# Performance work log

Measured on AMD Instinct MI355X. Metric: run time of the kernel, lower is better.

Reference implementation:

```python
import jax, jax.numpy as jnp
import numpy as np

TABLE_NUM = 16
TABLE_SIZE_LOG2 = 12
T = 1 << TABLE_SIZE_LOG2          # 4096 entries per table
FEAT = 2                          # features per entry (mini_linear in = table_num*2)
Z_DIM = 512
RES_MIN = 16
RES_MAX = 256
IMG = 256
MLP_HIDDEN = 64
OUT_DIM = 3
BATCH = 8
PRIME_Y = np.uint32(2654435761)   # instant-NGP spatial hash prime


def setup_inputs() -> dict:
    key = jax.random.key(0)
    ks = jax.random.split(key, 9)
    d_tab = TABLE_NUM * T * FEAT
    return {
        "z": jax.random.normal(ks[0], (BATCH, Z_DIM), jnp.float32),
        "w_table": jax.random.normal(ks[1], (Z_DIM, d_tab), jnp.float32) * 1e-2,
        "b_table": jnp.zeros((d_tab,), jnp.float32),
        "w1": jax.random.normal(ks[2], (TABLE_NUM * FEAT, MLP_HIDDEN), jnp.float32) * (1.0 / np.sqrt(TABLE_NUM * FEAT)),
        "b1": jnp.zeros((MLP_HIDDEN,), jnp.float32),
        "w2": jax.random.normal(ks[3], (MLP_HIDDEN, MLP_HIDDEN), jnp.float32) * (1.0 / np.sqrt(MLP_HIDDEN)),
        "b2": jnp.zeros((MLP_HIDDEN,), jnp.float32),
        "w3": jax.random.normal(ks[4], (MLP_HIDDEN, OUT_DIM), jnp.float32) * (1.0 / np.sqrt(MLP_HIDDEN)),
        "b3": jnp.zeros((OUT_DIM,), jnp.float32),
    }


def _sample_coords(b):
    c = (jnp.arange(IMG, dtype=jnp.float32) + 0.5) / IMG
    xx, yy = jnp.meshgrid(c, c, indexing="ij")  # torch.meshgrid default
    coords = jnp.stack([xx, yy], axis=-1).reshape(1, -1, 2)
    return jnp.broadcast_to(coords, (b, IMG * IMG, 2))


def _hash_retrieve(tables, coords):
    """tables: B x L x T x F; coords: B x N x 2 in [0,1). Returns B x N x (L*F)."""
    B, L, _, _ = tables.shape
    growth = np.exp((np.log(RES_MAX) - np.log(RES_MIN)) / (L - 1))
    offs = jnp.array([[0, 0], [1, 0], [0, 1], [1, 1]], dtype=jnp.uint32)  # 4 corners
    bidx = jnp.arange(B)[:, None, None]
    feats = []
    for l in range(L):
        res = jnp.float32(RES_MIN * (growth ** l))
        pos = coords * res                      # B,N,2
        pos0 = jnp.floor(pos)
        frac = pos - pos0                       # B,N,2
        corner = pos0.astype(jnp.uint32)[:, :, None, :] + offs[None, None]  # B,N,4,2
        idx = (corner[..., 0] ^ (corner[..., 1] * PRIME_Y)) & jnp.uint32(T - 1)
        f = tables[:, l][bidx, idx.astype(jnp.int32)]        # B,N,4,F gather
        fx, fy = frac[..., 0], frac[..., 1]
        w = jnp.stack([(1 - fx) * (1 - fy), fx * (1 - fy),
                       (1 - fx) * fy,       fx * fy], axis=-1)  # B,N,4
        feats.append(jnp.einsum("bncf,bnc->bnf", f, w))
    return jnp.concatenate(feats, axis=-1)


def reference(z, w_table, b_table, w1, b1, w2, b2, w3, b3):
    B = z.shape[0]
    tables = (z @ w_table + b_table).reshape(B, TABLE_NUM, T, FEAT)
    coords = _sample_coords(B).astype(tables.dtype)
    feat = _hash_retrieve(tables, coords)                    # B,N,L*F
    h = jax.nn.relu(feat @ w1 + b1)
    h = jax.nn.relu(h @ w2 + b2)
    o = jnp.tanh(h @ w3 + b3)                                # B,N,3
    return o.reshape(B, IMG, IMG, OUT_DIM).transpose(0, 3, 1, 2)
```

## Files before the change

kernel.cpp:

```cpp
#include <hip/hip_runtime.h>
#include <cmath>

#define TABLE_NUM 16
#define T_SIZE    4096
#define Z_DIM     512
#define IMG       256
#define D_TAB     (TABLE_NUM * T_SIZE * 2)
#define BATCH     8
#define HID       64
#define N_PIX     (IMG * IMG)
#define PRIME_Y   2654435761u
#define KCHUNK    4
#define KLEN      (Z_DIM / KCHUNK)
#define NG4       (D_TAB / 4)

typedef _Float16 v8h  __attribute__((ext_vector_type(8)));
typedef _Float16 v2h  __attribute__((ext_vector_type(2)));
typedef float    v4f  __attribute__((ext_vector_type(4)));

struct ResArr { float r[TABLE_NUM]; };

__device__ constexpr int WCAP[16]  = {3,4,4,4,5,5,5,6,7,8,9,10,11,13,15,18};
__device__ constexpr int CBASE[16] = {0,9,25,41,57,82,107,132,168,217,281,362,462,583,752,977};
#define CTOT 1301

__global__ void prep_weights(const float* __restrict__ w1, const float* __restrict__ w2,
                             const float* __restrict__ w3, const float* __restrict__ z,
                             _Float16* __restrict__ w1T, _Float16* __restrict__ w2T,
                             _Float16* __restrict__ w3T, float* __restrict__ zT)
{
    const int t = threadIdx.x;
    for (int i = t; i < HID * 32; i += 256) {
        int n = i >> 5, k = i & 31;
        w1T[i] = (_Float16)w1[k * HID + n];
    }
    for (int i = t; i < HID * HID; i += 256) {
        int n = i >> 6, k = i & 63;
        w2T[i] = (_Float16)w2[k * HID + n];
    }
    for (int i = t; i < 16 * HID; i += 256) {
        int n = i >> 6, k = i & 63;
        w3T[i] = (_Float16)(n < 3 ? w3[k * 3 + n] : 0.f);
    }
    for (int i = t; i < Z_DIM * BATCH; i += 256) {
        int k = i >> 3, b = i & 7;
        zT[i] = z[b * Z_DIM + k];
    }
}

__global__ __launch_bounds__(256) void gen_partial(
    const float* __restrict__ zT, const float* __restrict__ w,
    float* __restrict__ part)
{
    const int c  = blockIdx.x >> 7;
    const int g  = (blockIdx.x & 127) * 256 + threadIdx.x;
    const int k0 = c * KLEN;
    const float4* wp = reinterpret_cast<const float4*>(w) + g;

    float4 acc[BATCH];
#pragma unroll
    for (int b = 0; b < BATCH; ++b) acc[b] = make_float4(0.f, 0.f, 0.f, 0.f);

#pragma unroll 8
    for (int kk = 0; kk < KLEN; ++kk) {
        const int k = k0 + kk;
        float4 wv = wp[(size_t)k * NG4];
        const float* zr = zT + k * BATCH;
#pragma unroll
        for (int b = 0; b < BATCH; ++b) {
            float zv = zr[b];
            acc[b].x = fmaf(zv, wv.x, acc[b].x);
            acc[b].y = fmaf(zv, wv.y, acc[b].y);
            acc[b].z = fmaf(zv, wv.z, acc[b].z);
            acc[b].w = fmaf(zv, wv.w, acc[b].w);
        }
    }

    float4* pp = reinterpret_cast<float4*>(part);
#pragma unroll
    for (int b = 0; b < BATCH; ++b)
        pp[((size_t)(c * BATCH + b) << 15) + g] = acc[b];
}

__global__ __launch_bounds__(256) void gen_reduce(
    const float* __restrict__ part, const float* __restrict__ bt,
    float* __restrict__ tabs)
{
    const int i = blockIdx.x * 256 + threadIdx.x;
    const int b = i >> 15, g = i & (NG4 - 1);
    const float4* pp = reinterpret_cast<const float4*>(part);

    float4 s = pp[((size_t)b << 15) + g];
#pragma unroll
    for (int c = 1; c < KCHUNK; ++c) {
        float4 p = pp[((size_t)(c * BATCH + b) << 15) + g];
        s.x += p.x; s.y += p.y; s.z += p.z; s.w += p.w;
    }
    float4 bv = reinterpret_cast<const float4*>(bt)[g];
    s.x += bv.x; s.y += bv.y; s.z += bv.z; s.w += bv.w;
    reinterpret_cast<float4*>(tabs)[((size_t)b << 15) + g] = s;
}

__global__ __launch_bounds__(256) void hash_mlp(
    const float* __restrict__ tabs,
    const _Float16* __restrict__ w1T, const _Float16* __restrict__ w2T,
    const _Float16* __restrict__ w3T,
    const float* __restrict__ b1, const float* __restrict__ b2,
    const float* __restrict__ b3,
    float* __restrict__ out, ResArr res)
{
    __shared__ _Float16 mbuf[4][64][72];
    __shared__ float2   cstage[CTOT];

    const int tid  = threadIdx.x;
    const int wid  = tid >> 6;
    const int lane = tid & 63;
    const int b    = blockIdx.x & 7;
    const int tile = blockIdx.x >> 3;
    const int i0b  = (tile >> 4) * 16;
    const int j0b  = (tile & 15) * 16;
    const int i0   = i0b + wid * 4;

    const int di = lane >> 4, dj = lane & 15;
    const float cxp = ((float)(i0 + di) + 0.5f) * (1.0f / IMG);
    const float cyp = ((float)(j0b + dj) + 0.5f) * (1.0f / IMG);
    const float2* tb2 = reinterpret_cast<const float2*>(tabs + (size_t)b * D_TAB);

    const float cx_lo = ((float)i0b + 0.5f) * (1.0f / IMG);
    const float cy_lo = ((float)j0b + 0.5f) * (1.0f / IMG);

#pragma unroll
    for (int l = 0; l < TABLE_NUM; ++l) {
        const float r  = res.r[l];
        const int   xs = (int)floorf(cx_lo * r);
        const int   ys = (int)floorf(cy_lo * r);
        const float2* tl = tb2 + l * T_SIZE;
        const int W = WCAP[l], CNT = WCAP[l] * WCAP[l];
        for (int e = tid; e < CNT; e += 256) {
            int yy = e / W, xx = e - yy * W;
            unsigned idx = ((unsigned)(xs + xx) ^
                            ((unsigned)(ys + yy) * PRIME_Y)) & (T_SIZE - 1);
            cstage[CBASE[l] + e] = tl[idx];
        }
    }
    __syncthreads();

#pragma unroll
    for (int l = 0; l < TABLE_NUM; ++l) {
        const float r   = res.r[l];
        const float xsf = floorf(cx_lo * r);
        const float ysf = floorf(cy_lo * r);
        float px = cxp * r, py = cyp * r;
        float fx0 = floorf(px), fy0 = floorf(py);
        float fx = px - fx0, fy = py - fy0;
        int xi = (int)(fx0 - xsf), yi = (int)(fy0 - ysf);
        const float2* cb = cstage + CBASE[l];
        const int W = WCAP[l];
        float2 f00 = cb[yi * W + xi];
        float2 f10 = cb[yi * W + xi + 1];
        float2 f01 = cb[(yi + 1) * W + xi];
        float2 f11 = cb[(yi + 1) * W + xi + 1];
        float w00 = (1.f - fx) * (1.f - fy);
        float w10 = fx * (1.f - fy);
        float w01 = (1.f - fx) * fy;
        float w11 = fx * fy;
        float e0 = f00.x * w00 + f10.x * w10 + f01.x * w01 + f11.x * w11;
        float e1 = f00.y * w00 + f10.y * w10 + f01.y * w01 + f11.y * w11;
        v2h p; p.x = (_Float16)e0; p.y = (_Float16)e1;
        *reinterpret_cast<v2h*>(&mbuf[wid][lane][2 * l]) = p;
    }

    const int arow = lane & 15;
    const int kgrp = lane >> 4;

    float bias1v[4], bias2v[4];
#pragma unroll
    for (int nt = 0; nt < 4; ++nt) {
        bias1v[nt] = b1[nt * 16 + arow];
        bias2v[nt] = b2[nt * 16 + arow];
    }
    const float bias3 = (arow < 3) ? b3[arow] : 0.f;

    v8h bf1[4], bf2a[4], bf2b[4];
#pragma unroll
    for (int nt = 0; nt < 4; ++nt) {
        bf1[nt]  = *reinterpret_cast<const v8h*>(&w1T[(nt * 16 + arow) * 32 + kgrp * 8]);
        bf2a[nt] = *reinterpret_cast<const v8h*>(&w2T[(nt * 16 + arow) * 64 + kgrp * 8]);
        bf2b[nt] = *reinterpret_cast<const v8h*>(&w2T[(nt * 16 + arow) * 64 + 32 + kgrp * 8]);
    }
    v8h bf3a = *reinterpret_cast<const v8h*>(&w3T[arow * 64 + kgrp * 8]);
    v8h bf3b = *reinterpret_cast<const v8h*>(&w3T[arow * 64 + 32 + kgrp * 8]);

    v8h a1[4];
#pragma unroll
    for (int mt = 0; mt < 4; ++mt)
        a1[mt] = *reinterpret_cast<const v8h*>(&mbuf[wid][mt * 16 + arow][kgrp * 8]);

    v4f c1[4][4];
#pragma unroll
    for (int nt = 0; nt < 4; ++nt)
#pragma unroll
        for (int mt = 0; mt < 4; ++mt) {
            v4f c = {0.f, 0.f, 0.f, 0.f};
            c = __builtin_amdgcn_mfma_f32_16x16x32_f16(a1[mt], bf1[nt], c, 0, 0, 0);
#pragma unroll
            for (int e = 0; e < 4; ++e)
                c1[mt][nt][e] = fmaxf(c[e] + bias1v[nt], 0.f);
        }

#pragma unroll
    for (int mt = 0; mt < 4; ++mt)
#pragma unroll
        for (int nt = 0; nt < 4; ++nt)
#pragma unroll
            for (int e = 0; e < 4; ++e)
                mbuf[wid][mt * 16 + kgrp * 4 + e][nt * 16 + arow] = (_Float16)c1[mt][nt][e];

    v8h a2[4][2];
#pragma unroll
    for (int mt = 0; mt < 4; ++mt) {
        a2[mt][0] = *reinterpret_cast<const v8h*>(&mbuf[wid][mt * 16 + arow][kgrp * 8]);
        a2[mt][1] = *reinterpret_cast<const v8h*>(&mbuf[wid][mt * 16 + arow][32 + kgrp * 8]);
    }
    v4f c2[4][4];
#pragma unroll
    for (int nt = 0; nt < 4; ++nt)
#pragma unroll
        for (int mt = 0; mt < 4; ++mt) {
            v4f c = {0.f, 0.f, 0.f, 0.f};
            c = __builtin_amdgcn_mfma_f32_16x16x32_f16(a2[mt][0], bf2a[nt], c, 0, 0, 0);
            c = __builtin_amdgcn_mfma_f32_16x16x32_f16(a2[mt][1], bf2b[nt], c, 0, 0, 0);
#pragma unroll
            for (int e = 0; e < 4; ++e)
                c2[mt][nt][e] = fmaxf(c[e] + bias2v[nt], 0.f);
        }

#pragma unroll
    for (int mt = 0; mt < 4; ++mt)
#pragma unroll
        for (int nt = 0; nt < 4; ++nt)
#pragma unroll
            for (int e = 0; e < 4; ++e)
                mbuf[wid][mt * 16 + kgrp * 4 + e][nt * 16 + arow] = (_Float16)c2[mt][nt][e];

#pragma unroll
    for (int mt = 0; mt < 4; ++mt) {
        v8h a0  = *reinterpret_cast<const v8h*>(&mbuf[wid][mt * 16 + arow][kgrp * 8]);
        v8h a1v = *reinterpret_cast<const v8h*>(&mbuf[wid][mt * 16 + arow][32 + kgrp * 8]);
        v4f c = {0.f, 0.f, 0.f, 0.f};
        c = __builtin_amdgcn_mfma_f32_16x16x32_f16(a0,  bf3a, c, 0, 0, 0);
        c = __builtin_amdgcn_mfma_f32_16x16x32_f16(a1v, bf3b, c, 0, 0, 0);
        if (arow < 3) {
            float4 st;
            st.x = tanhf(c[0] + bias3);
            st.y = tanhf(c[1] + bias3);
            st.z = tanhf(c[2] + bias3);
            st.w = tanhf(c[3] + bias3);
            size_t idx = ((size_t)b * 3 + arow) * N_PIX
                       + (size_t)(i0 + mt) * IMG + j0b + kgrp * 4;
            *reinterpret_cast<float4*>(&out[idx]) = st;
        }
    }
}

extern "C" void kernel_launch(void* const* d_in, const int* in_sizes, int n_in,
                              void* d_out, int out_size, void* d_ws, size_t ws_size,
                              hipStream_t stream)
{
    const float* z  = (const float*)d_in[0];
    const float* wt = (const float*)d_in[1];
    const float* bt = (const float*)d_in[2];
    const float* w1 = (const float*)d_in[3];
    const float* b1 = (const float*)d_in[4];
    const float* w2 = (const float*)d_in[5];
    const float* b2 = (const float*)d_in[6];
    const float* w3 = (const float*)d_in[7];
    const float* b3 = (const float*)d_in[8];
    float* out  = (float*)d_out;

    char* ws = (char*)d_ws;
    float*     tabs = (float*)ws;
    float*     part = (float*)(ws + (4 << 20));
    _Float16*  w1T  = (_Float16*)(ws + (20 << 20));
    _Float16*  w2T  = (_Float16*)(ws + (20 << 20) + 4096);
    _Float16*  w3T  = (_Float16*)(ws + (20 << 20) + 12288);
    float*     zT   = (float*)(ws + (20 << 20) + 16384);

    ResArr ra;
    const double growth = std::exp((std::log(256.0) - std::log(16.0)) / 15.0);
    for (int l = 0; l < TABLE_NUM; ++l)
        ra.r[l] = (float)(16.0 * std::pow(growth, (double)l));

    prep_weights<<<1, 256, 0, stream>>>(w1, w2, w3, z, w1T, w2T, w3T, zT);
    gen_partial<<<KCHUNK * (NG4 / 256), 256, 0, stream>>>(zT, wt, part);
    gen_reduce<<<BATCH * NG4 / 256, 256, 0, stream>>>(part, bt, tabs);
    hash_mlp<<<BATCH * (N_PIX / 256), 256, 0, stream>>>(
        tabs, w1T, w2T, w3T, b1, b2, b3, out, ra);
}
```

Baseline: 99.41 us.

## Shrink hash_mlp tiles and swap MFMA operand roles with register shuffles

Each block now covers a 4x16 pixel tile, and each wave handles one 16-pixel row, so the grid is four times larger. The staged corner region is sized per level with separate x and y widths, which shrinks shared memory to a small cstage buffer. The MLP is rewritten to use weights as the A operand and per-pixel features as B. Intermediate activations move between layers through ds_bpermute in registers rather than an LDS mbuf round-trip. This removes the large shared buffer and its traffic, which should raise occupancy. The cost is more redundant table gathers across the smaller tiles, repeated weight loads per wave, and narrower scalar output stores.

After: 129.8 us. +30.6%, slower.

```diff
diff --git a/kernel.cpp b/kernel.cpp
--- a/kernel.cpp
+++ b/kernel.cpp
@@ -20,9 +20,15 @@
 
 struct ResArr { float r[TABLE_NUM]; };
 
-__device__ constexpr int WCAP[16]  = {3,4,4,4,5,5,5,6,7,8,9,10,11,13,15,18};
-__device__ constexpr int CBASE[16] = {0,9,25,41,57,82,107,132,168,217,281,362,462,583,752,977};
-#define CTOT 1301
+__device__ constexpr int XW[16]    = {3,3,3,3,3,3,3,3,3,4,4,4,5,5,5,6};
+__device__ constexpr int YW[16]    = {3,4,4,4,5,5,5,6,7,8,9,10,11,13,15,18};
+__device__ constexpr int CBASE[16] = {0,9,21,33,45,60,75,90,108,129,161,197,237,292,357,432};
+#define CTOT 540
+
+__device__ __forceinline__ int pkf16(float a, float b) {
+    v2h p; p.x = (_Float16)a; p.y = (_Float16)b;
+    int r; __builtin_memcpy(&r, &p, 4); return r;
+}
 
 __global__ void prep_weights(const float* __restrict__ w1, const float* __restrict__ w2,
                              const float* __restrict__ w3, const float* __restrict__ z,
@@ -109,23 +115,19 @@
     const float* __restrict__ b3,
     float* __restrict__ out, ResArr res)
 {
-    __shared__ _Float16 mbuf[4][64][72];
-    __shared__ float2   cstage[CTOT];
+    __shared__ float2 cstage[CTOT];
 
     const int tid  = threadIdx.x;
-    const int wid  = tid >> 6;
+    const int w    = tid >> 6;
     const int lane = tid & 63;
+    const int g    = lane >> 4;
+    const int arow = lane & 15;
     const int b    = blockIdx.x & 7;
     const int tile = blockIdx.x >> 3;
-    const int i0b  = (tile >> 4) * 16;
+    const int i0b  = (tile >> 4) * 4;
     const int j0b  = (tile & 15) * 16;
-    const int i0   = i0b + wid * 4;
-
-    const int di = lane >> 4, dj = lane & 15;
-    const float cxp = ((float)(i0 + di) + 0.5f) * (1.0f / IMG);
-    const float cyp = ((float)(j0b + dj) + 0.5f) * (1.0f / IMG);
+
     const float2* tb2 = reinterpret_cast<const float2*>(tabs + (size_t)b * D_TAB);
-
     const float cx_lo = ((float)i0b + 0.5f) * (1.0f / IMG);
     const float cy_lo = ((float)j0b + 0.5f) * (1.0f / IMG);
 
@@ -134,131 +136,133 @@
         const float r  = res.r[l];
         const int   xs = (int)floorf(cx_lo * r);
         const int   ys = (int)floorf(cy_lo * r);
-        const float2* tl = tb2 + l * T_SIZE;
-        const int W = WCAP[l], CNT = WCAP[l] * WCAP[l];
-        for (int e = tid; e < CNT; e += 256) {
-            int yy = e / W, xx = e - yy * W;
+        const int   Wl = XW[l], CNT = XW[l] * YW[l];
+        if (tid < CNT) {
+            int yy = tid / Wl, xx = tid - yy * Wl;
             unsigned idx = ((unsigned)(xs + xx) ^
                             ((unsigned)(ys + yy) * PRIME_Y)) & (T_SIZE - 1);
-            cstage[CBASE[l] + e] = tl[idx];
+            cstage[CBASE[l] + tid] = tb2[l * T_SIZE + idx];
         }
     }
     __syncthreads();
 
-#pragma unroll
-    for (int l = 0; l < TABLE_NUM; ++l) {
-        const float r   = res.r[l];
-        const float xsf = floorf(cx_lo * r);
-        const float ysf = floorf(cy_lo * r);
+    const int ii = i0b + w;
+    const int jj = j0b + arow;
+    const float cxp = ((float)ii + 0.5f) * (1.0f / IMG);
+    const float cyp = ((float)jj + 0.5f) * (1.0f / IMG);
+
+    v8h bfeat;
+#pragma unroll
+    for (int fi = 0; fi < 4; ++fi) {
+        const float r  = g == 0 ? res.r[fi]     : g == 1 ? res.r[4 + fi]
+                       : g == 2 ? res.r[8 + fi] : res.r[12 + fi];
+        const int  Wl  = g == 0 ? XW[fi]        : g == 1 ? XW[4 + fi]
+                       : g == 2 ? XW[8 + fi]    : XW[12 + fi];
+        const int  bas = g == 0 ? CBASE[fi]     : g == 1 ? CBASE[4 + fi]
+                       : g == 2 ? CBASE[8 + fi] : CBASE[12 + fi];
+        float xsf = floorf(cx_lo * r), ysf = floorf(cy_lo * r);
         float px = cxp * r, py = cyp * r;
         float fx0 = floorf(px), fy0 = floorf(py);
         float fx = px - fx0, fy = py - fy0;
         int xi = (int)(fx0 - xsf), yi = (int)(fy0 - ysf);
-        const float2* cb = cstage + CBASE[l];
-        const int W = WCAP[l];
-        float2 f00 = cb[yi * W + xi];
-        float2 f10 = cb[yi * W + xi + 1];
-        float2 f01 = cb[(yi + 1) * W + xi];
-        float2 f11 = cb[(yi + 1) * W + xi + 1];
+        const float2* cb = cstage + bas;
+        float2 f00 = cb[yi * Wl + xi];
+        float2 f10 = cb[yi * Wl + xi + 1];
+        float2 f01 = cb[(yi + 1) * Wl + xi];
+        float2 f11 = cb[(yi + 1) * Wl + xi + 1];
         float w00 = (1.f - fx) * (1.f - fy);
         float w10 = fx * (1.f - fy);
         float w01 = (1.f - fx) * fy;
         float w11 = fx * fy;
         float e0 = f00.x * w00 + f10.x * w10 + f01.x * w01 + f11.x * w11;
         float e1 = f00.y * w00 + f10.y * w10 + f01.y * w01 + f11.y * w11;
-        v2h p; p.x = (_Float16)e0; p.y = (_Float16)e1;
-        *reinterpret_cast<v2h*>(&mbuf[wid][lane][2 * l]) = p;
-    }
-
-    const int arow = lane & 15;
-    const int kgrp = lane >> 4;
-
-    float bias1v[4], bias2v[4];
-#pragma unroll
-    for (int nt = 0; nt < 4; ++nt) {
-        bias1v[nt] = b1[nt * 16 + arow];
-        bias2v[nt] = b2[nt * 16 + arow];
-    }
-    const float bias3 = (arow < 3) ? b3[arow] : 0.f;
-
-    v8h bf1[4], bf2a[4], bf2b[4];
-#pragma unroll
-    for (int nt = 0; nt < 4; ++nt) {
-        bf1[nt]  = *reinterpret_cast<const v8h*>(&w1T[(nt * 16 + arow) * 32 + kgrp * 8]);
-        bf2a[nt] = *reinterpret_cast<const v8h*>(&w2T[(nt * 16 + arow) * 64 + kgrp * 8]);
-        bf2b[nt] = *reinterpret_cast<const v8h*>(&w2T[(nt * 16 + arow) * 64 + 32 + kgrp * 8]);
-    }
-    v8h bf3a = *reinterpret_cast<const v8h*>(&w3T[arow * 64 + kgrp * 8]);
-    v8h bf3b = *reinterpret_cast<const v8h*>(&w3T[arow * 64 + 32 + kgrp * 8]);
-
-    v8h a1[4];
-#pragma unroll
-    for (int mt = 0; mt < 4; ++mt)
-        a1[mt] = *reinterpret_cast<const v8h*>(&mbuf[wid][mt * 16 + arow][kgrp * 8]);
-
-    v4f c1[4][4];
-#pragma unroll
-    for (int nt = 0; nt < 4; ++nt)
-#pragma unroll
-        for (int mt = 0; mt < 4; ++mt) {
-            v4f c = {0.f, 0.f, 0.f, 0.f};
-            c = __builtin_amdgcn_mfma_f32_16x16x32_f16(a1[mt], bf1[nt], c, 0, 0, 0);
-#pragma unroll
-            for (int e = 0; e < 4; ++e)
-                c1[mt][nt][e] = fmaxf(c[e] + bias1v[nt], 0.f);
-        }
-
-#pragma unroll
-    for (int mt = 0; mt < 4; ++mt)
-#pragma unroll
-        for (int nt = 0; nt < 4; ++nt)
-#pragma unroll
-            for (int e = 0; e < 4; ++e)
-                mbuf[wid][mt * 16 + kgrp * 4 + e][nt * 16 + arow] = (_Float16)c1[mt][nt][e];
-
-    v8h a2[4][2];
+        bfeat[2 * fi]     = (_Float16)e0;
+        bfeat[2 * fi + 1] = (_Float16)e1;
+    }
+
+    const int idx0 = ((((2 * g + 0) & 3) << 4) | arow) << 2;
+    const int idx1 = ((((2 * g + 1) & 3) << 4) | arow) << 2;
+    const bool ghi = (g >= 2);
+
+    v4f c1[4];
 #pragma unroll
     for (int mt = 0; mt < 4; ++mt) {
-        a2[mt][0] = *reinterpret_cast<const v8h*>(&mbuf[wid][mt * 16 + arow][kgrp * 8]);
-        a2[mt][1] = *reinterpret_cast<const v8h*>(&mbuf[wid][mt * 16 + arow][32 + kgrp * 8]);
-    }
-    v4f c2[4][4];
-#pragma unroll
-    for (int nt = 0; nt < 4; ++nt)
-#pragma unroll
-        for (int mt = 0; mt < 4; ++mt) {
-            v4f c = {0.f, 0.f, 0.f, 0.f};
-            c = __builtin_amdgcn_mfma_f32_16x16x32_f16(a2[mt][0], bf2a[nt], c, 0, 0, 0);
-            c = __builtin_amdgcn_mfma_f32_16x16x32_f16(a2[mt][1], bf2b[nt], c, 0, 0, 0);
-#pragma unroll
-            for (int e = 0; e < 4; ++e)
-                c2[mt][nt][e] = fmaxf(c[e] + bias2v[nt], 0.f);
-        }
-
-#pragma unroll
-    for (int mt = 0; mt < 4; ++mt)
-#pragma unroll
-        for (int nt = 0; nt < 4; ++nt)
-#pragma unroll
-            for (int e = 0; e < 4; ++e)
-                mbuf[wid][mt * 16 + kgrp * 4 + e][nt * 16 + arow] = (_Float16)c2[mt][nt][e];
-
+        v8h wa = *reinterpret_cast<const v8h*>(&w1T[(mt * 16 + arow) * 32 + g * 8]);
+        v4f c = {0.f, 0.f, 0.f, 0.f};
+        c = __builtin_amdgcn_mfma_f32_16x16x32_f16(wa, bfeat, c, 0, 0, 0);
+        float4 bv = *reinterpret_cast<const float4*>(&b1[mt * 16 + g * 4]);
+        c1[mt][0] = fmaxf(c[0] + bv.x, 0.f);
+        c1[mt][1] = fmaxf(c[1] + bv.y, 0.f);
+        c1[mt][2] = fmaxf(c[2] + bv.z, 0.f);
+        c1[mt][3] = fmaxf(c[3] + bv.w, 0.f);
+    }
+
+    int pk1[4][2];
 #pragma unroll
     for (int mt = 0; mt < 4; ++mt) {
-        v8h a0  = *reinterpret_cast<const v8h*>(&mbuf[wid][mt * 16 + arow][kgrp * 8]);
-        v8h a1v = *reinterpret_cast<const v8h*>(&mbuf[wid][mt * 16 + arow][32 + kgrp * 8]);
+        pk1[mt][0] = pkf16(c1[mt][0], c1[mt][1]);
+        pk1[mt][1] = pkf16(c1[mt][2], c1[mt][3]);
+    }
+    v8h bB2[2];
+#pragma unroll
+    for (int kc = 0; kc < 2; ++kc) {
+        int t[4];
+#pragma unroll
+        for (int d = 0; d < 4; ++d) {
+            int idx = (d >> 1) ? idx1 : idx0;
+            int lo = __builtin_amdgcn_ds_bpermute(idx, pk1[2 * kc][d & 1]);
+            int hi = __builtin_amdgcn_ds_bpermute(idx, pk1[2 * kc + 1][d & 1]);
+            t[d] = ghi ? hi : lo;
+        }
+        __builtin_memcpy(&bB2[kc], t, 16);
+    }
+
+    v4f c2[4];
+#pragma unroll
+    for (int mt = 0; mt < 4; ++mt) {
+        v8h wa0 = *reinterpret_cast<const v8h*>(&w2T[(mt * 16 + arow) * 64 + g * 8]);
+        v8h wa1 = *reinterpret_cast<const v8h*>(&w2T[(mt * 16 + arow) * 64 + 32 + g * 8]);
         v4f c = {0.f, 0.f, 0.f, 0.f};
-        c = __builtin_amdgcn_mfma_f32_16x16x32_f16(a0,  bf3a, c, 0, 0, 0);
-        c = __builtin_amdgcn_mfma_f32_16x16x32_f16(a1v, bf3b, c, 0, 0, 0);
-        if (arow < 3) {
-            float4 st;
-            st.x = tanhf(c[0] + bias3);
-            st.y = tanhf(c[1] + bias3);
-            st.z = tanhf(c[2] + bias3);
-            st.w = tanhf(c[3] + bias3);
-            size_t idx = ((size_t)b * 3 + arow) * N_PIX
-                       + (size_t)(i0 + mt) * IMG + j0b + kgrp * 4;
-            *reinterpret_cast<float4*>(&out[idx]) = st;
+        c = __builtin_amdgcn_mfma_f32_16x16x32_f16(wa0, bB2[0], c, 0, 0, 0);
+        c = __builtin_amdgcn_mfma_f32_16x16x32_f16(wa1, bB2[1], c, 0, 0, 0);
+        float4 bv = *reinterpret_cast<const float4*>(&b2[mt * 16 + g * 4]);
+        c2[mt][0] = fmaxf(c[0] + bv.x, 0.f);
+        c2[mt][1] = fmaxf(c[1] + bv.y, 0.f);
+        c2[mt][2] = fmaxf(c[2] + bv.z, 0.f);
+        c2[mt][3] = fmaxf(c[3] + bv.w, 0.f);
+    }
+
+    int pk2[4][2];
+#pragma unroll
+    for (int mt = 0; mt < 4; ++mt) {
+        pk2[mt][0] = pkf16(c2[mt][0], c2[mt][1]);
+        pk2[mt][1] = pkf16(c2[mt][2], c2[mt][3]);
+    }
+    v8h bB3[2];
+#pragma unroll
+    for (int kc = 0; kc < 2; ++kc) {
+        int t[4];
+#pragma unroll
+        for (int d = 0; d < 4; ++d) {
+            int idx = (d >> 1) ? idx1 : idx0;
+            int lo = __builtin_amdgcn_ds_bpermute(idx, pk2[2 * kc][d & 1]);
+            int hi = __builtin_amdgcn_ds_bpermute(idx, pk2[2 * kc + 1][d & 1]);
+            t[d] = ghi ? hi : lo;
+        }
+        __builtin_memcpy(&bB3[kc], t, 16);
+    }
+
+    v8h w3a = *reinterpret_cast<const v8h*>(&w3T[arow * 64 + g * 8]);
+    v8h w3b = *reinterpret_cast<const v8h*>(&w3T[arow * 64 + 32 + g * 8]);
+    v4f c3 = {0.f, 0.f, 0.f, 0.f};
+    c3 = __builtin_amdgcn_mfma_f32_16x16x32_f16(w3a, bB3[0], c3, 0, 0, 0);
+    c3 = __builtin_amdgcn_mfma_f32_16x16x32_f16(w3b, bB3[1], c3, 0, 0, 0);
+
+    if (g == 0) {
+#pragma unroll
+        for (int e = 0; e < 3; ++e) {
+            float o = tanhf(c3[e] + b3[e]);
+            out[((size_t)(b * 3 + e)) * N_PIX + (size_t)ii * IMG + jj] = o;
         }
     }
 }
@@ -294,6 +298,6 @@
     prep_weights<<<1, 256, 0, stream>>>(w1, w2, w3, z, w1T, w2T, w3T, zT);
     gen_partial<<<KCHUNK * (NG4 / 256), 256, 0, stream>>>(zT, wt, part);
     gen_reduce<<<BATCH * NG4 / 256, 256, 0, stream>>>(part, bt, tabs);
-    hash_mlp<<<BATCH * (N_PIX / 256), 256, 0, stream>>>(
+    hash_mlp<<<BATCH * (N_PIX / 64), 256, 0, stream>>>(
         tabs, w1T, w2T, w3T, b1, b2, b3, out, ra);
 }
```
